# Optimization experiments

Measured on AMD Instinct MI355X. Metric: run time of the kernel, lower is better.

## Reference

```python
import jax, jax.numpy as jnp
import numpy as np

B, N, W, C = 32, 2048, 64, 1024  # batch, memory_size, word_size, controller_size
EPS = 1e-8


def setup_inputs() -> dict:
    key = jax.random.key(0)
    ks = jax.random.split(key, 10)
    s = 0.02
    return {
        "controller_output": jax.random.normal(ks[0], (B, C), jnp.float32),
        "prev_read_weights": jax.random.uniform(ks[1], (B, N), jnp.float32),
        "prev_write_weight": jax.random.uniform(ks[2], (B, N), jnp.float32),
        "memory": jax.random.normal(ks[3], (B, N, W), jnp.float32),
        "usage": jax.random.uniform(ks[4], (B, N), jnp.float32),
        "Wk": (jax.random.normal(ks[5], (W, C), jnp.float32) * s), "bk": jnp.zeros((W,), jnp.float32),
        "Wb": (jax.random.normal(ks[6], (1, C), jnp.float32) * s), "bb": jnp.zeros((1,), jnp.float32),
        "Ws": (jax.random.normal(ks[7], (3, C), jnp.float32) * s), "bs": jnp.zeros((3,), jnp.float32),
        "Wg": (jax.random.normal(ks[8], (1, C), jnp.float32) * s), "bg": jnp.zeros((1,), jnp.float32),
    }


def reference(controller_output, prev_read_weights, prev_write_weight, memory, usage,
              Wk, bk, Wb, bb, Ws, bs, Wg, bg):
    # --- content addressing ---
    k = jnp.tanh(controller_output @ Wk.T + bk)                     # [B, W]
    beta = jax.nn.softplus(controller_output @ Wb.T + bb)[:, 0]     # [B]
    sim = jnp.einsum('bnw,bw->bn', memory, k)                       # [B, N]
    content_weights = jax.nn.softmax(sim * beta[:, None], axis=-1)  # [B, N]

    # --- shift-matrix directional addressing ---
    shift = jax.nn.softmax(controller_output @ Ws.T + bs, axis=-1)  # [B, 3]
    sc = (-shift[:, 0] + shift[:, 2])[:, None, None]                # [B, 1, 1]
    idx = jnp.arange(N, dtype=jnp.float32)
    dist = (idx[:, None] - idx[None, :] + N / 2) % N                # [N, N]
    kernel = jnp.exp(-(dist[None] ** 2) / (2.0 * sc ** 2 + EPS))    # [B, N, N]
    kernel = kernel / (kernel.sum(axis=2, keepdims=True) + EPS)
    directional_weights = jnp.einsum('bn,bnm->bm', prev_read_weights, kernel)  # [B, N]

    # --- allocation: sort usage, cumprod of (1-usage), scatter back ---
    order = jnp.argsort(usage, axis=-1)                             # [B, N]
    sorted_usage = jnp.take_along_axis(usage, order, axis=-1)
    cumprod = jnp.cumprod(1.0 - sorted_usage, axis=-1)
    brow = jnp.arange(usage.shape[0])[:, None]
    allocation_weights = jnp.zeros_like(usage).at[brow, order].set(cumprod)

    # --- combine ---
    write_gate = jax.nn.sigmoid(controller_output @ Wg.T + bg)[:, 0]  # [B]
    write_weights = write_gate[:, None] * (
        0.5 * content_weights + 0.5 * directional_weights * allocation_weights)
    return (write_weights, content_weights, directional_weights, allocation_weights)
```

## Files before the change

### kernel.cpp

```cpp
#include <hip/hip_runtime.h>

#define BB 32
#define NN 2048
#define WW 64
#define CC 1024
#define NTAP 17
#define NB 512
#define EPSF 1e-8f

#define WS_X 0
#define WS_Q (BB*NN)
#define WS_P (2*BB*NN)
#define WS_G (2*BB*NN + BB*4)

__global__ __launch_bounds__(1024) void k1(
    const float* __restrict__ co, const float* __restrict__ rdw,
    const float* __restrict__ usage, const float* __restrict__ mem,
    const float* __restrict__ Wk, const float* __restrict__ bk,
    const float* __restrict__ Wb, const float* __restrict__ bb,
    const float* __restrict__ Ws, const float* __restrict__ bs,
    const float* __restrict__ Wg, const float* __restrict__ bg,
    float* __restrict__ ws, float* __restrict__ out)
{
    __shared__ float co_s[CC];
    __shared__ __align__(16) float k_s[WW + 4];
    __shared__ float r_s[NN];
    __shared__ unsigned long long skey[NN];
    __shared__ float slog[NN];
    __shared__ float alloc_s[NN];
    __shared__ unsigned hist[NB];
    __shared__ float binlog[NB];
    __shared__ unsigned binStart[NB];
    __shared__ unsigned cursor[NB];
    __shared__ float binpre[NB];
    __shared__ unsigned uw[8];
    __shared__ float fw[8];
    __shared__ float dot4[16][4];
    __shared__ float sred[16];
    __shared__ float scalars[8];
    __shared__ float wd_s[NTAP];

    const int tid = threadIdx.x, wave = tid >> 6, lane = tid & 63;

    if (blockIdx.x < BB) {
        const int b = blockIdx.x;
        if (tid < NB) { hist[tid] = 0u; binlog[tid] = 0.f; }
        co_s[tid] = co[(size_t)b * CC + tid];
        r_s[tid]        = rdw[(size_t)b * NN + tid];
        r_s[tid + 1024] = rdw[(size_t)b * NN + tid + 1024];
        float u0 = usage[(size_t)b * NN + tid];
        float u1 = usage[(size_t)b * NN + tid + 1024];
        __syncthreads();
        float lg0 = __logf(1.0f - u0), lg1 = __logf(1.0f - u1);
        int bin0 = (int)(u0 * NB); bin0 = bin0 < 0 ? 0 : (bin0 > NB - 1 ? NB - 1 : bin0);
        int bin1 = (int)(u1 * NB); bin1 = bin1 < 0 ? 0 : (bin1 > NB - 1 ? NB - 1 : bin1);
        atomicAdd(&hist[bin0], 1u); atomicAdd(&binlog[bin0], lg0);
        atomicAdd(&hist[bin1], 1u); atomicAdd(&binlog[bin1], lg1);
        {
            float cv = co_s[tid];
            float p0 = cv * Ws[tid], p1 = cv * Ws[CC + tid],
                  p2 = cv * Ws[2 * CC + tid], p3 = cv * Wg[tid];
            #pragma unroll
            for (int off = 32; off; off >>= 1) {
                p0 += __shfl_xor(p0, off); p1 += __shfl_xor(p1, off);
                p2 += __shfl_xor(p2, off); p3 += __shfl_xor(p3, off);
            }
            if (lane == 0) {
                dot4[wave][0] = p0; dot4[wave][1] = p1;
                dot4[wave][2] = p2; dot4[wave][3] = p3;
            }
        }
        __syncthreads();
        unsigned hv = 0u; float bv = 0.f, fi = 0.f; unsigned ui = 0u;
        if (tid < NB) {
            hv = hist[tid]; bv = binlog[tid];
            ui = hv; fi = bv;
            #pragma unroll
            for (int off = 1; off < 64; off <<= 1) {
                unsigned tu = __shfl_up(ui, off);
                float    tf = __shfl_up(fi, off);
                if (lane >= off) { ui += tu; fi += tf; }
            }
            if (lane == 63) { uw[wave] = ui; fw[wave] = fi; }
        }
        if (tid < 4) {
            float s = 0.f;
            #pragma unroll
            for (int w = 0; w < 16; w++) s += dot4[w][tid];
            scalars[tid] = s + ((tid < 3) ? bs[tid] : bg[0]);
        }
        __syncthreads();
        if (tid < 8) {
            unsigned v = uw[tid]; float f = fw[tid];
            #pragma unroll
            for (int off = 1; off < 8; off <<= 1) {
                unsigned tu = __shfl_up(v, off);
                float    tf = __shfl_up(f, off);
                if (tid >= off) { v += tu; f += tf; }
            }
            uw[tid] = v; fw[tid] = f;
        } else if (tid == 16) {
            float g = scalars[3];
            float gate = 1.f / (1.f + __expf(-g));
            scalars[6] = gate;
            ws[WS_G + b] = gate;
            float s0 = scalars[0], s1 = scalars[1], s2 = scalars[2];
            float m = fmaxf(s0, fmaxf(s1, s2));
            float e0 = __expf(s0 - m), e1 = __expf(s1 - m), e2 = __expf(s2 - m);
            float inv = 1.f / (e0 + e1 + e2);
            float sc = (e2 - e0) * inv;
            float den = 2.f * sc * sc + EPSF;
            float w[NTAP]; float S = 0.f;
            #pragma unroll
            for (int d = 0; d < NTAP; d++) { w[d] = __expf(-(float)(d * d) / den); S += w[d]; }
            float invS = 1.f / (S + EPSF);
            #pragma unroll
            for (int d = 0; d < NTAP; d++) wd_s[d] = w[d] * invS;
        }
        __syncthreads();
        if (tid < NB) {
            unsigned woff = wave ? uw[wave - 1] : 0u;
            float    foff = wave ? fw[wave - 1] : 0.f;
            unsigned st = woff + ui - hv;
            binStart[tid] = st; cursor[tid] = st;
            binpre[tid] = foff + fi - bv;
        }
        __syncthreads();
        unsigned long long key0 = ((unsigned long long)__float_as_uint(u0) << 32) | (unsigned)tid;
        unsigned long long key1 = ((unsigned long long)__float_as_uint(u1) << 32) | (unsigned)(tid + 1024);
        {
            unsigned p0 = atomicAdd(&cursor[bin0], 1u);
            skey[p0] = key0; slog[p0] = lg0;
            unsigned p1 = atomicAdd(&cursor[bin1], 1u);
            skey[p1] = key1; slog[p1] = lg1;
        }
        __syncthreads();
        float* aout = out + 3 * (size_t)BB * NN + (size_t)b * NN;
        #pragma unroll
        for (int pp = 0; pp < 2; pp++) {
            int p = tid + pp * 1024;
            unsigned long long kp = skey[p];
            float up = __uint_as_float((unsigned)(kp >> 32));
            int c = (int)(up * NB); c = c < 0 ? 0 : (c > NB - 1 ? NB - 1 : c);
            unsigned st = binStart[c], cnt = hist[c];
            float s = binpre[c];
            for (unsigned q = 0; q < cnt; q++)
                s += (skey[st + q] <= kp) ? slog[st + q] : 0.f;
            float a = __expf(s);
            unsigned oidx = (unsigned)(kp & 0xFFFFFFFFu);
            alloc_s[oidx] = a;
            aout[oidx] = a;
        }
        __syncthreads();
        const float gate = scalars[6];
        float dw0 = 0.f, dw1 = 0.f;
        #pragma unroll
        for (int d = 0; d < NTAP; d++) {
            float w = wd_s[d];
            dw0 = fmaf(w, r_s[(tid + 1024 + d) & (NN - 1)], dw0);
            dw1 = fmaf(w, r_s[(tid + d) & (NN - 1)], dw1);
        }
        out[2 * (size_t)BB * NN + (size_t)b * NN + tid]        = dw0;
        out[2 * (size_t)BB * NN + (size_t)b * NN + tid + 1024] = dw1;
        ws[WS_Q + (size_t)b * NN + tid]        = 0.5f * gate * dw0 * alloc_s[tid];
        ws[WS_Q + (size_t)b * NN + tid + 1024] = 0.5f * gate * dw1 * alloc_s[tid + 1024];
    } else {
        const int i = blockIdx.x - BB;
        const int b = i >> 2, j = i & 3;
        const int base = j * 512;
        co_s[tid] = co[(size_t)b * CC + tid];
        __syncthreads();
        const float4* co4 = reinterpret_cast<const float4*>(co_s);
        #pragma unroll
        for (int rr = 0; rr < 4; ++rr) {
            const int o = wave + rr * 16;
            const float4* wrow = reinterpret_cast<const float4*>(Wk + (size_t)o * CC);
            float s = 0.f;
            #pragma unroll
            for (int ch = 0; ch < 4; ++ch) {
                float4 wv = wrow[ch * 64 + lane];
                float4 cv = co4[ch * 64 + lane];
                s += wv.x * cv.x + wv.y * cv.y + wv.z * cv.z + wv.w * cv.w;
            }
            #pragma unroll
            for (int off = 32; off; off >>= 1) s += __shfl_xor(s, off);
            if (lane == 0) k_s[o] = tanhf(s + bk[o]);
        }
        if (wave == 0) {
            const float4* wrow = reinterpret_cast<const float4*>(Wb);
            float s = 0.f;
            #pragma unroll
            for (int ch = 0; ch < 4; ++ch) {
                float4 wv = wrow[ch * 64 + lane];
                float4 cv = co4[ch * 64 + lane];
                s += wv.x * cv.x + wv.y * cv.y + wv.z * cv.z + wv.w * cv.w;
            }
            #pragma unroll
            for (int off = 32; off; off >>= 1) s += __shfl_xor(s, off);
            if (lane == 0) k_s[WW] = s + bb[0];
        }
        __syncthreads();
        const float xb = k_s[WW];
        const float beta = (xb > 20.f) ? xb : log1pf(__expf(xb));
        const int lane16 = tid & 15, group = tid >> 4;
        const float4 k4 = reinterpret_cast<const float4*>(k_s)[lane16];
        float4 mr[8];
        #pragma unroll
        for (int it = 0; it < 8; ++it) {
            const int row = base + it * 64 + group;
            mr[it] = *reinterpret_cast<const float4*>(
                mem + ((size_t)b * NN + row) * WW + lane16 * 4);
        }
        float esum = 0.f;
        #pragma unroll
        for (int it = 0; it < 8; ++it) {
            const int row = base + it * 64 + group;
            float s = mr[it].x * k4.x + mr[it].y * k4.y
                    + mr[it].z * k4.z + mr[it].w * k4.w;
            s += __shfl_xor(s, 1); s += __shfl_xor(s, 2);
            s += __shfl_xor(s, 4); s += __shfl_xor(s, 8);
            if (lane16 == 0) {
                float e = __expf(s * beta);
                ws[WS_X + (size_t)b * NN + row] = e;
                esum += e;
            }
        }
        #pragma unroll
        for (int off = 32; off; off >>= 1) esum += __shfl_xor(esum, off);
        if (lane == 0) sred[wave] = esum;
        __syncthreads();
        if (tid < 16) {
            float v = sred[tid];
            v += __shfl_xor(v, 1); v += __shfl_xor(v, 2);
            v += __shfl_xor(v, 4); v += __shfl_xor(v, 8);
            if (tid == 0) ws[WS_P + (size_t)b * 4 + j] = v;
        }
    }
}

__global__ __launch_bounds__(1024) void k2(const float* __restrict__ ws,
                                           float* __restrict__ out)
{
    const int bid = blockIdx.x, b = bid >> 1, half = bid & 1;
    const int n = half * 1024 + threadIdx.x;
    const float* part = ws + WS_P + (size_t)b * 4;
    const float D = part[0] + part[1] + part[2] + part[3];
    const float invd = 1.f / D;
    const float gate = ws[WS_G + b];
    const float c = ws[WS_X + (size_t)b * NN + n] * invd;
    out[(size_t)BB * NN + (size_t)b * NN + n] = c;
    out[(size_t)b * NN + n] = fmaf(0.5f * gate, c, ws[WS_Q + (size_t)b * NN + n]);
}

extern "C" void kernel_launch(void* const* d_in, const int* in_sizes, int n_in,
                              void* d_out, int out_size, void* d_ws, size_t ws_size,
                              hipStream_t stream) {
    const float* co    = (const float*)d_in[0];
    const float* rdw   = (const float*)d_in[1];
    const float* mem   = (const float*)d_in[3];
    const float* usage = (const float*)d_in[4];
    const float* Wk    = (const float*)d_in[5];
    const float* bk    = (const float*)d_in[6];
    const float* Wb    = (const float*)d_in[7];
    const float* bb    = (const float*)d_in[8];
    const float* Ws_   = (const float*)d_in[9];
    const float* bs    = (const float*)d_in[10];
    const float* Wg    = (const float*)d_in[11];
    const float* bg    = (const float*)d_in[12];
    float* out = (float*)d_out;
    float* wsf = (float*)d_ws;

    hipLaunchKernelGGL(k1, dim3(BB + 128), dim3(1024), 0, stream,
                       co, rdw, usage, mem, Wk, bk, Wb, bb, Ws_, bs, Wg, bg,
                       wsf, out);
    hipLaunchKernelGGL(k2, dim3(2 * BB), dim3(1024), 0, stream, wsf, out);
}
```

Baseline: 18.03 us.

## Fuse two kernels into one using global flag-based inter-block synchronization

Merges the finalize kernel into the main kernel. Content-softmax blocks publish partial sums with release flags, then spin-wait for sibling partials and for the allocation block's flag before writing final outputs. Unnormalized exponentials stay in shared memory instead of a workspace round trip. This removes a launch and a global store/load pass. It relies on all blocks being co-resident, and the flags are never reset between calls, which risks reading stale data on repeated invocations.

```diff
diff --git a/kernel.cpp b/kernel.cpp
--- a/kernel.cpp
+++ b/kernel.cpp
@@ -7,13 +7,15 @@
 #define NTAP 17
 #define NB 512
 #define EPSF 1e-8f
-
-#define WS_X 0
-#define WS_Q (BB*NN)
-#define WS_P (2*BB*NN)
-#define WS_G (2*BB*NN + BB*4)
-
-__global__ __launch_bounds__(1024) void k1(
+#define TOKEN 0x5A5A5A5Au
+
+#define WS_Q  0
+#define WS_P  (BB*NN)
+#define WS_G  (BB*NN + BB*4)
+#define WS_FA (BB*NN + BB*5)
+#define WS_FS (BB*NN + BB*6)
+
+__global__ __launch_bounds__(1024) void k_one(
     const float* __restrict__ co, const float* __restrict__ rdw,
     const float* __restrict__ usage, const float* __restrict__ mem,
     const float* __restrict__ Wk, const float* __restrict__ bk,
@@ -39,11 +41,15 @@
     __shared__ float sred[16];
     __shared__ float scalars[8];
     __shared__ float wd_s[NTAP];
+    __shared__ float bcast[2];
 
     const int tid = threadIdx.x, wave = tid >> 6, lane = tid & 63;
-
-    if (blockIdx.x < BB) {
-        const int b = blockIdx.x;
+    const int bid = blockIdx.x;
+    unsigned* flagA = (unsigned*)(ws + WS_FA);
+    unsigned* flagS = (unsigned*)(ws + WS_FS);
+
+    if (bid < BB) {
+        const int b = bid;
         if (tid < NB) { hist[tid] = 0u; binlog[tid] = 0.f; }
         co_s[tid] = co[(size_t)b * CC + tid];
         r_s[tid]        = rdw[(size_t)b * NN + tid];
@@ -103,7 +109,8 @@
             float g = scalars[3];
             float gate = 1.f / (1.f + __expf(-g));
             scalars[6] = gate;
-            ws[WS_G + b] = gate;
+            __hip_atomic_store(ws + WS_G + b, gate,
+                               __ATOMIC_RELAXED, __HIP_MEMORY_SCOPE_AGENT);
             float s0 = scalars[0], s1 = scalars[1], s2 = scalars[2];
             float m = fmaxf(s0, fmaxf(s1, s2));
             float e0 = __expf(s0 - m), e1 = __expf(s1 - m), e2 = __expf(s2 - m);
@@ -164,8 +171,14 @@
         out[2 * (size_t)BB * NN + (size_t)b * NN + tid + 1024] = dw1;
         ws[WS_Q + (size_t)b * NN + tid]        = 0.5f * gate * dw0 * alloc_s[tid];
         ws[WS_Q + (size_t)b * NN + tid + 1024] = 0.5f * gate * dw1 * alloc_s[tid + 1024];
+        __syncthreads();
+        if (tid == 0) {
+            __threadfence();
+            __hip_atomic_store(&flagA[b], TOKEN,
+                               __ATOMIC_RELEASE, __HIP_MEMORY_SCOPE_AGENT);
+        }
     } else {
-        const int i = blockIdx.x - BB;
+        const int i = bid - BB;
         const int b = i >> 2, j = i & 3;
         const int base = j * 512;
         co_s[tid] = co[(size_t)b * CC + tid];
@@ -214,14 +227,13 @@
         float esum = 0.f;
         #pragma unroll
         for (int it = 0; it < 8; ++it) {
-            const int row = base + it * 64 + group;
             float s = mr[it].x * k4.x + mr[it].y * k4.y
                     + mr[it].z * k4.z + mr[it].w * k4.w;
             s += __shfl_xor(s, 1); s += __shfl_xor(s, 2);
             s += __shfl_xor(s, 4); s += __shfl_xor(s, 8);
             if (lane16 == 0) {
                 float e = __expf(s * beta);
-                ws[WS_X + (size_t)b * NN + row] = e;
+                slog[it * 64 + group] = e;
                 esum += e;
             }
         }
@@ -229,27 +241,47 @@
         for (int off = 32; off; off >>= 1) esum += __shfl_xor(esum, off);
         if (lane == 0) sred[wave] = esum;
         __syncthreads();
-        if (tid < 16) {
-            float v = sred[tid];
-            v += __shfl_xor(v, 1); v += __shfl_xor(v, 2);
-            v += __shfl_xor(v, 4); v += __shfl_xor(v, 8);
-            if (tid == 0) ws[WS_P + (size_t)b * 4 + j] = v;
+        if (tid == 0) {
+            float v = 0.f;
+            #pragma unroll
+            for (int w = 0; w < 16; w++) v += sred[w];
+            __hip_atomic_store(ws + WS_P + (size_t)b * 4 + j, v,
+                               __ATOMIC_RELAXED, __HIP_MEMORY_SCOPE_AGENT);
+            __hip_atomic_store(&flagS[b * 4 + j], TOKEN,
+                               __ATOMIC_RELEASE, __HIP_MEMORY_SCOPE_AGENT);
+        }
+        if (tid < 3) {
+            const int s = (j + 1 + tid) & 3;
+            while (__hip_atomic_load(&flagS[b * 4 + s],
+                                     __ATOMIC_ACQUIRE, __HIP_MEMORY_SCOPE_AGENT) != TOKEN)
+                __builtin_amdgcn_s_sleep(8);
+        } else if (tid == 3) {
+            while (__hip_atomic_load(&flagA[b],
+                                     __ATOMIC_ACQUIRE, __HIP_MEMORY_SCOPE_AGENT) != TOKEN)
+                __builtin_amdgcn_s_sleep(8);
+        }
+        __syncthreads();
+        if (tid == 0) {
+            float D = 0.f;
+            #pragma unroll
+            for (int s = 0; s < 4; ++s)
+                D += __hip_atomic_load(ws + WS_P + (size_t)b * 4 + s,
+                                       __ATOMIC_RELAXED, __HIP_MEMORY_SCOPE_AGENT);
+            bcast[0] = 1.f / D;
+            bcast[1] = __hip_atomic_load(ws + WS_G + b,
+                                         __ATOMIC_RELAXED, __HIP_MEMORY_SCOPE_AGENT);
+        }
+        __syncthreads();
+        const float invD = bcast[0], gate = bcast[1];
+        if (tid < 512) {
+            const int n = base + tid;
+            const float qv = __hip_atomic_load(ws + WS_Q + (size_t)b * NN + n,
+                                               __ATOMIC_RELAXED, __HIP_MEMORY_SCOPE_AGENT);
+            const float c = slog[tid] * invD;
+            out[(size_t)BB * NN + (size_t)b * NN + n] = c;
+            out[(size_t)b * NN + n] = fmaf(0.5f * gate, c, qv);
         }
     }
-}
-
-__global__ __launch_bounds__(1024) void k2(const float* __restrict__ ws,
-                                           float* __restrict__ out)
-{
-    const int bid = blockIdx.x, b = bid >> 1, half = bid & 1;
-    const int n = half * 1024 + threadIdx.x;
-    const float* part = ws + WS_P + (size_t)b * 4;
-    const float D = part[0] + part[1] + part[2] + part[3];
-    const float invd = 1.f / D;
-    const float gate = ws[WS_G + b];
-    const float c = ws[WS_X + (size_t)b * NN + n] * invd;
-    out[(size_t)BB * NN + (size_t)b * NN + n] = c;
-    out[(size_t)b * NN + n] = fmaf(0.5f * gate, c, ws[WS_Q + (size_t)b * NN + n]);
 }
 
 extern "C" void kernel_launch(void* const* d_in, const int* in_sizes, int n_in,
@@ -270,8 +302,7 @@
     float* out = (float*)d_out;
     float* wsf = (float*)d_ws;
 
-    hipLaunchKernelGGL(k1, dim3(BB + 128), dim3(1024), 0, stream,
+    hipLaunchKernelGGL(k_one, dim3(BB + 128), dim3(1024), 0, stream,
                        co, rdw, usage, mem, Wk, bk, Wb, bb, Ws_, bs, Wg, bg,
                        wsf, out);
-    hipLaunchKernelGGL(k2, dim3(2 * BB), dim3(1024), 0, stream, wsf, out);
 }
```

Result: slower. 20.90 us (+15.9%).
